# Performance work log

Hardware: AMD Instinct MI355X
Metric: run time of the kernel (lower is better)

## Reference

```python
import jax, jax.numpy as jnp
import numpy as np

C = 128; D_STATE = 16; D_CONV = 4; EXPAND = 2
DI = EXPAND * C          # 256 inner dim
DT_RANK = (C + 15) // 16 # 8
NM, T, V = 32, 64, 22


def _mamba(x, in_w, conv_w, conv_b, xproj_w, dt_w, dt_b, Alog, Dp, out_w):
    """Standard Mamba block. x: (B, L, C) -> (B, L, C)."""
    B_, L, _ = x.shape
    xz = x @ in_w.T                       # (B, L, 2*DI)
    xi, z = jnp.split(xz, 2, axis=-1)     # each (B, L, DI)
    # causal depthwise conv over L, kernel D_CONV
    K = conv_w.shape[-1]
    xp = jnp.pad(xi, ((0, 0), (K - 1, 0), (0, 0)))
    xc = conv_b + sum(xp[:, k:k + L, :] * conv_w[:, k] for k in range(K))
    xc = jax.nn.silu(xc)
    dbl = xc @ xproj_w.T                  # (B, L, DT_RANK + 2*D_STATE)
    dt, Bm, Cm = jnp.split(dbl, [DT_RANK, DT_RANK + D_STATE], axis=-1)
    dt = jax.nn.softplus(dt @ dt_w.T + dt_b)   # (B, L, DI)
    A = -jnp.exp(Alog)                    # (DI, D_STATE), strictly negative

    def step(h, inp):
        dt_l, B_l, C_l, u_l = inp         # (B,DI) (B,DS) (B,DS) (B,DI)
        dA = jnp.exp(dt_l[:, :, None] * A)             # (B, DI, DS)
        h = dA * h + (dt_l * u_l)[:, :, None] * B_l[:, None, :]
        y = jnp.einsum('bds,bs->bd', h, C_l)
        return h, y

    h0 = jnp.zeros((B_, DI, D_STATE), x.dtype)
    xs = (jnp.moveaxis(dt, 1, 0), jnp.moveaxis(Bm, 1, 0),
          jnp.moveaxis(Cm, 1, 0), jnp.moveaxis(xc, 1, 0))
    _, ys = jax.lax.scan(step, h0, xs)    # ys: (L, B, DI)
    y = jnp.moveaxis(ys, 0, 1) + xc * Dp  # skip connection
    y = y * jax.nn.silu(z)
    return y @ out_w.T                    # (B, L, C)


def setup_inputs() -> dict:
    key = jax.random.key(0)
    ks = jax.random.split(key, 40)
    i = [0]
    def nrm(shape, s=0.05):
        i[0] += 1
        return jax.random.normal(ks[i[0]], shape, jnp.float32) * s
    inp = {"x": jax.random.normal(ks[0], (NM, C, T, V), jnp.float32)}
    for p in ("f", "b"):
        inp[p + "_in_w"] = nrm((2 * DI, C))
        inp[p + "_conv_w"] = nrm((DI, D_CONV), 0.2)
        inp[p + "_conv_b"] = nrm((DI,))
        inp[p + "_xproj_w"] = nrm((DT_RANK + 2 * D_STATE, DI))
        inp[p + "_dt_w"] = nrm((DI, DT_RANK), 0.1)
        inp[p + "_dt_b"] = nrm((DI,), 0.1)
        i[0] += 1
        inp[p + "_Alog"] = jax.random.uniform(ks[i[0]], (DI, D_STATE), jnp.float32)
        inp[p + "_D"] = nrm((DI,), 1.0)
        inp[p + "_out_w"] = nrm((C, DI))
    inp["fuse_w"] = nrm((C, 2 * C))
    inp["ln_w"] = jnp.ones((C,), jnp.float32)
    inp["ln_b"] = jnp.zeros((C,), jnp.float32)
    return inp


def reference(x, f_in_w, f_conv_w, f_conv_b, f_xproj_w, f_dt_w, f_dt_b, f_Alog, f_D, f_out_w,
              b_in_w, b_conv_w, b_conv_b, b_xproj_w, b_dt_w, b_dt_b, b_Alog, b_D, b_out_w,
              fuse_w, ln_w, ln_b):
    nm, c, t, v = x.shape
    xs = jnp.transpose(x, (0, 2, 3, 1)).reshape(nm * t, v, c)   # (B, V, C)
    fwd = _mamba(xs, f_in_w, f_conv_w, f_conv_b, f_xproj_w, f_dt_w, f_dt_b, f_Alog, f_D, f_out_w)
    bwd = _mamba(xs[:, ::-1, :], b_in_w, b_conv_w, b_conv_b, b_xproj_w, b_dt_w, b_dt_b, b_Alog, b_D, b_out_w)[:, ::-1, :]
    y = jnp.concatenate([fwd, bwd], axis=-1) @ fuse_w.T         # (B, V, C)
    mu = y.mean(-1, keepdims=True)
    var = y.var(-1, keepdims=True)
    y = (y - mu) / jnp.sqrt(var + 1e-5) * ln_w + ln_b
    return jnp.transpose(y.reshape(nm, t, v, c), (0, 3, 1, 2))  # (NM, C, T, V)
```

## Files before the change

### kernel.cpp

```cpp
#include <hip/hip_runtime.h>
#include <hip/hip_bf16.h>
#include <math.h>

namespace {

typedef unsigned short u16;
typedef unsigned int u32;

constexpr int LSEQ = 22, CD = 128, DI = 256, TDIM = 64;

constexpr int XS_LD = 136;
constexpr int XI_LD = 264;
constexpr int Z_LD  = 264;
constexpr int Y2_LD = 132;

constexpr int O_DT0 = 0;
constexpr int O_DT1 = 352;
constexpr int O_BC0 = 704;
constexpr int O_BC1 = 2112;
constexpr int O_XS  = 0;
constexpr int O_XI0 = 3520;
constexpr int O_XI1 = 9328;
constexpr int O_Z0  = 15136;
constexpr int O_Z1  = 20944;
constexpr int POOLN = 26752;

constexpr int WS_F_IN_HI = 0;
constexpr int WS_F_IN_LO = 65536;
constexpr int WS_B_IN_HI = 131072;
constexpr int WS_B_IN_LO = 196608;
constexpr int WS_F_OUT   = 262144;
constexpr int WS_B_OUT   = 294912;
constexpr int WS_FUSE    = 327680;
constexpr int WS_F_XP_HI = 360448;
constexpr int WS_F_XP_LO = 372736;
constexpr int WS_B_XP_HI = 385024;
constexpr int WS_B_XP_LO = 397312;
constexpr int WS_TOTAL   = 409600;

typedef __attribute__((ext_vector_type(8))) short bf16x8;
typedef __attribute__((ext_vector_type(4))) float f32x4;

__device__ __forceinline__ u16 f2bf(float f) {
  __bf16 b = (__bf16)f;
  return *reinterpret_cast<u16*>(&b);
}
__device__ __forceinline__ float bf2f(u16 h) {
  return __uint_as_float(((u32)h) << 16);
}
__device__ __forceinline__ float sigm(float x) { return 1.0f / (1.0f + __expf(-x)); }

__global__ void prep_weights(const float* __restrict__ f_in, const float* __restrict__ b_in,
                             const float* __restrict__ f_xp, const float* __restrict__ b_xp,
                             u16* __restrict__ ws) {
  int i = blockIdx.x * 256 + threadIdx.x;
  if (i >= WS_TOTAL) return;
  u16 r = 0;
  if (i < WS_F_IN_LO) {
    r = f2bf(f_in[i]);
  } else if (i < WS_B_IN_HI) {
    float v = f_in[i - WS_F_IN_LO];
    r = f2bf(v - bf2f(f2bf(v)));
  } else if (i < WS_B_IN_LO) {
    r = f2bf(b_in[i - WS_B_IN_HI]);
  } else if (i < WS_F_OUT) {
    float v = b_in[i - WS_B_IN_LO];
    r = f2bf(v - bf2f(f2bf(v)));
  } else if (i < WS_F_XP_HI) {
    r = 0;
  } else if (i < WS_F_XP_LO) {
    int j = i - WS_F_XP_HI, n = j >> 8, k = j & 255;
    r = (n < 40) ? f2bf(f_xp[n * 256 + k]) : (u16)0;
  } else if (i < WS_B_XP_HI) {
    int j = i - WS_F_XP_LO, n = j >> 8, k = j & 255;
    if (n < 40) { float v = f_xp[n * 256 + k]; r = f2bf(v - bf2f(f2bf(v))); } else r = 0;
  } else if (i < WS_B_XP_LO) {
    int j = i - WS_B_XP_HI, n = j >> 8, k = j & 255;
    r = (n < 40) ? f2bf(b_xp[n * 256 + k]) : (u16)0;
  } else {
    int j = i - WS_B_XP_LO, n = j >> 8, k = j & 255;
    if (n < 40) { float v = b_xp[n * 256 + k]; r = f2bf(v - bf2f(f2bf(v))); } else r = 0;
  }
  ws[i] = r;
}

__global__ void prep_fold(const float* __restrict__ f_out, const float* __restrict__ b_out,
                          const float* __restrict__ fuse, u16* __restrict__ ws) {
  int i = blockIdx.x * 256 + threadIdx.x;
  int half = i >> 15;
  int j = i & 32767;
  int c = j >> 8, d = j & 255;
  const float* ow = half ? b_out : f_out;
  const float* fw = fuse + c * 256 + half * 128;
  float acc = 0.f;
#pragma unroll 4
  for (int k = 0; k < 128; ++k) acc = fmaf(fw[k], ow[k * 256 + d], acc);
  ws[(half ? WS_B_OUT : WS_F_OUT) + c * 256 + d] = f2bf(acc);
}

__global__ __launch_bounds__(512, 4) void spatial_mamba_kernel(
    const float* __restrict__ x,
    const float* __restrict__ f_conv_w, const float* __restrict__ f_conv_b,
    const float* __restrict__ f_dt_w, const float* __restrict__ f_dt_b,
    const float* __restrict__ f_Alog, const float* __restrict__ f_D,
    const float* __restrict__ b_conv_w, const float* __restrict__ b_conv_b,
    const float* __restrict__ b_dt_w, const float* __restrict__ b_dt_b,
    const float* __restrict__ b_Alog, const float* __restrict__ b_D,
    const float* __restrict__ ln_w, const float* __restrict__ ln_b,
    const u16* __restrict__ ws,
    float* __restrict__ out)
{
  __shared__ __align__(16) u16 pool[POOLN];

  u16* xs = pool + O_XS;
  float* y2 = (float*)(pool + O_Z0);
  float* mu_s = (float*)pool;
  float* rs_s = mu_s + LSEQ;

  const int tid = threadIdx.x;
  const int wv = tid >> 6, ln = tid & 63, lr = ln & 15, lg = ln >> 4;
  const int blk = blockIdx.x;
  const int nm = blk / TDIM, t = blk - nm * TDIM;
  const size_t base = (size_t)nm * CD * (TDIM * LSEQ) + (size_t)t * LSEQ;

  const int ra0 = (lr < LSEQ) ? lr : (LSEQ - 1);
  const int ra1 = (16 + lr < LSEQ) ? (16 + lr) : (LSEQ - 1);
  const int rb0 = (LSEQ - 1) - lr;
  const int rb1 = (lr < 6) ? (5 - lr) : 0;

  for (int idx = tid; idx < LSEQ * CD; idx += 512) {
    int c = idx / LSEQ, v = idx - c * LSEQ;
    xs[v * XS_LD + c] = f2bf(x[base + (size_t)c * (TDIM * LSEQ) + v]);
  }
  __syncthreads();

  {
    bf16x8 afr[2][4];
#pragma unroll
    for (int kt = 0; kt < 4; ++kt) {
      afr[0][kt] = *(const bf16x8*)&xs[ra0 * XS_LD + kt * 32 + lg * 8];
      afr[1][kt] = *(const bf16x8*)&xs[ra1 * XS_LD + kt * 32 + lg * 8];
    }
#pragma unroll
    for (int dir = 0; dir < 2; ++dir) {
      const u16* ih = ws + (dir ? WS_B_IN_HI : WS_F_IN_HI);
      const u16* il = ws + (dir ? WS_B_IN_LO : WS_F_IN_LO);
      f32x4 acc[2][4];
#pragma unroll
      for (int m = 0; m < 2; ++m)
#pragma unroll
        for (int n = 0; n < 4; ++n) acc[m][n] = f32x4{0.f, 0.f, 0.f, 0.f};
#pragma unroll
      for (int kt = 0; kt < 4; ++kt) {
#pragma unroll
        for (int n = 0; n < 4; ++n) {
          const int off = (wv * 64 + n * 16 + lr) * 128 + kt * 32 + lg * 8;
          bf16x8 bh = *(const bf16x8*)(ih + off);
          bf16x8 bl = *(const bf16x8*)(il + off);
          acc[0][n] = __builtin_amdgcn_mfma_f32_16x16x32_bf16(afr[0][kt], bh, acc[0][n], 0, 0, 0);
          acc[0][n] = __builtin_amdgcn_mfma_f32_16x16x32_bf16(afr[0][kt], bl, acc[0][n], 0, 0, 0);
          acc[1][n] = __builtin_amdgcn_mfma_f32_16x16x32_bf16(afr[1][kt], bh, acc[1][n], 0, 0, 0);
          acc[1][n] = __builtin_amdgcn_mfma_f32_16x16x32_bf16(afr[1][kt], bl, acc[1][n], 0, 0, 0);
        }
      }
      u16* dst = pool + ((wv < 4) ? (dir ? O_XI1 : O_XI0) : (dir ? O_Z1 : O_Z0));
      const int cb = (wv & 3) * 64;
#pragma unroll
      for (int m = 0; m < 2; ++m)
#pragma unroll
        for (int n = 0; n < 4; ++n)
#pragma unroll
          for (int j = 0; j < 4; ++j) {
            int row = 16 * m + lg * 4 + j;
            if (row < LSEQ) {
              int rr = dir ? (LSEQ - 1 - row) : row;
              dst[rr * XI_LD + cb + n * 16 + lr] = f2bf(acc[m][n][j]);
            }
          }
    }
  }
  __syncthreads();

  {
    const int dir = tid >> 8, d = tid & 255;
    const float* cw = dir ? b_conv_w : f_conv_w;
    const float* cbp = dir ? b_conv_b : f_conv_b;
    u16* xiD = pool + (dir ? O_XI1 : O_XI0);
    float4 w4 = *(const float4*)(cw + d * 4);
    float bb = cbp[d];
    float w0 = 0.f, w1 = 0.f, w2 = 0.f;
#pragma unroll
    for (int l = 0; l < LSEQ; ++l) {
      float w3 = bf2f(xiD[l * XI_LD + d]);
      float a = fmaf(w0, w4.x, bb);
      a = fmaf(w1, w4.y, a);
      a = fmaf(w2, w4.z, a);
      a = fmaf(w3, w4.w, a);
      float s = a * sigm(a);
      xiD[l * XI_LD + d] = f2bf(s);
      w0 = w1; w1 = w2; w2 = w3;
    }
  }
  __syncthreads();

  for (int tt = wv; tt < 12; tt += 8) {
    const int dir = tt / 6, r = tt - dir * 6, mt = r / 3, nt = r - mt * 3;
    const u16* xph = ws + (dir ? WS_B_XP_HI : WS_F_XP_HI);
    const u16* xpl = ws + (dir ? WS_B_XP_LO : WS_F_XP_LO);
    const u16* xcD = pool + (dir ? O_XI1 : O_XI0);
    const int ra = (mt * 16 + lr < LSEQ) ? (mt * 16 + lr) : (LSEQ - 1);
    f32x4 acc = f32x4{0.f, 0.f, 0.f, 0.f};
    const u16* bh_p = xph + (nt * 16 + lr) * 256 + lg * 8;
    const u16* bl_p = xpl + (nt * 16 + lr) * 256 + lg * 8;
#pragma unroll
    for (int kt = 0; kt < 8; ++kt) {
      bf16x8 a  = *(const bf16x8*)&xcD[ra * XI_LD + kt * 32 + lg * 8];
      bf16x8 bh = *(const bf16x8*)(bh_p + kt * 32);
      bf16x8 bl = *(const bf16x8*)(bl_p + kt * 32);
      acc = __builtin_amdgcn_mfma_f32_16x16x32_bf16(a, bh, acc, 0, 0, 0);
      acc = __builtin_amdgcn_mfma_f32_16x16x32_bf16(a, bl, acc, 0, 0, 0);
    }
    const int col = nt * 16 + lr;
    float* dtD = ((float*)pool) + (dir ? (O_DT1 / 2) : 0);
    float* bcD = ((float*)pool) + (dir ? (O_BC1 / 2) : (O_BC0 / 2));
#pragma unroll
    for (int j = 0; j < 4; ++j) {
      int row = mt * 16 + lg * 4 + j;
      if (row < LSEQ) {
        if (col < 8) dtD[row * 8 + col] = acc[j];
        else if (col < 40) bcD[row * 32 + (col - 8)] = acc[j];
      }
    }
  }
  __syncthreads();

  {
    const int dir = tid >> 8, d = tid & 255;
    const float* dtw  = dir ? b_dt_w : f_dt_w;
    const float* dtb  = dir ? b_dt_b : f_dt_b;
    const float* Alog = dir ? b_Alog : f_Alog;
    const float* Dp   = dir ? b_D : f_D;
    const float* dtD  = ((const float*)pool) + (dir ? (O_DT1 / 2) : 0);
    const float* bcD  = ((const float*)pool) + (dir ? (O_BC1 / 2) : (O_BC0 / 2));
    const u16* zD  = pool + (dir ? O_Z1 : O_Z0);
    u16* yD = pool + (dir ? O_XI1 : O_XI0);

    float4 dw0 = *(const float4*)(dtw + d * 8);
    float4 dw1 = *(const float4*)(dtw + d * 8 + 4);
    const float dtbv = dtb[d];
    float Av[16];
#pragma unroll
    for (int s4 = 0; s4 < 4; ++s4) {
      float4 a = *(const float4*)(Alog + d * 16 + s4 * 4);
      Av[s4 * 4 + 0] = -__expf(a.x);
      Av[s4 * 4 + 1] = -__expf(a.y);
      Av[s4 * 4 + 2] = -__expf(a.z);
      Av[s4 * 4 + 3] = -__expf(a.w);
    }
    const float Dd = Dp[d];
    float h[16];
#pragma unroll
    for (int s = 0; s < 16; ++s) h[s] = 0.f;
    for (int l = 0; l < LSEQ; ++l) {
      float4 q0 = *(const float4*)(dtD + l * 8);
      float4 q1 = *(const float4*)(dtD + l * 8 + 4);
      float sdt = dtbv;
      sdt = fmaf(q0.x, dw0.x, sdt); sdt = fmaf(q0.y, dw0.y, sdt);
      sdt = fmaf(q0.z, dw0.z, sdt); sdt = fmaf(q0.w, dw0.w, sdt);
      sdt = fmaf(q1.x, dw1.x, sdt); sdt = fmaf(q1.y, dw1.y, sdt);
      sdt = fmaf(q1.z, dw1.z, sdt); sdt = fmaf(q1.w, dw1.w, sdt);
      float dtv = (sdt > 20.f) ? sdt : __logf(1.f + __expf(sdt));
      float u = bf2f(yD[l * XI_LD + d]);
      float du = dtv * u;
      float4 b0 = *(const float4*)(bcD + l * 32);
      float4 b1 = *(const float4*)(bcD + l * 32 + 4);
      float4 b2 = *(const float4*)(bcD + l * 32 + 8);
      float4 b3 = *(const float4*)(bcD + l * 32 + 12);
      float4 c0 = *(const float4*)(bcD + l * 32 + 16);
      float4 c1 = *(const float4*)(bcD + l * 32 + 20);
      float4 c2 = *(const float4*)(bcD + l * 32 + 24);
      float4 c3 = *(const float4*)(bcD + l * 32 + 28);
      float acc = 0.f;
#define SC(s, bv, cv) { float dA = __expf(dtv * Av[s]); \
      h[s] = fmaf(dA, h[s], du * (bv)); \
      acc = fmaf(h[s], (cv), acc); }
      SC(0, b0.x, c0.x) SC(1, b0.y, c0.y) SC(2, b0.z, c0.z) SC(3, b0.w, c0.w)
      SC(4, b1.x, c1.x) SC(5, b1.y, c1.y) SC(6, b1.z, c1.z) SC(7, b1.w, c1.w)
      SC(8, b2.x, c2.x) SC(9, b2.y, c2.y) SC(10, b2.z, c2.z) SC(11, b2.w, c2.w)
      SC(12, b3.x, c3.x) SC(13, b3.y, c3.y) SC(14, b3.z, c3.z) SC(15, b3.w, c3.w)
#undef SC
      float zv = bf2f(zD[l * Z_LD + d]);
      float yo = fmaf(u, Dd, acc) * zv * sigm(zv);
      yD[l * XI_LD + d] = f2bf(yo);
    }
  }
  __syncthreads();

  {
    f32x4 acc[2] = {f32x4{0.f, 0.f, 0.f, 0.f}, f32x4{0.f, 0.f, 0.f, 0.f}};
    {
      const u16* wp = ws + WS_F_OUT;
      const u16* yD = pool + O_XI0;
#pragma unroll
      for (int kt = 0; kt < 8; ++kt) {
        bf16x8 b  = *(const bf16x8*)(wp + (wv * 16 + lr) * 256 + kt * 32 + lg * 8);
        bf16x8 a0 = *(const bf16x8*)&yD[ra0 * XI_LD + kt * 32 + lg * 8];
        bf16x8 a1 = *(const bf16x8*)&yD[ra1 * XI_LD + kt * 32 + lg * 8];
        acc[0] = __builtin_amdgcn_mfma_f32_16x16x32_bf16(a0, b, acc[0], 0, 0, 0);
        acc[1] = __builtin_amdgcn_mfma_f32_16x16x32_bf16(a1, b, acc[1], 0, 0, 0);
      }
    }
    {
      const u16* wp = ws + WS_B_OUT;
      const u16* yD = pool + O_XI1;
#pragma unroll
      for (int kt = 0; kt < 8; ++kt) {
        bf16x8 b  = *(const bf16x8*)(wp + (wv * 16 + lr) * 256 + kt * 32 + lg * 8);
        bf16x8 a0 = *(const bf16x8*)&yD[rb0 * XI_LD + kt * 32 + lg * 8];
        bf16x8 a1 = *(const bf16x8*)&yD[rb1 * XI_LD + kt * 32 + lg * 8];
        acc[0] = __builtin_amdgcn_mfma_f32_16x16x32_bf16(a0, b, acc[0], 0, 0, 0);
        acc[1] = __builtin_amdgcn_mfma_f32_16x16x32_bf16(a1, b, acc[1], 0, 0, 0);
      }
    }
#pragma unroll
    for (int m = 0; m < 2; ++m)
#pragma unroll
      for (int j = 0; j < 4; ++j) {
        int row = 16 * m + lg * 4 + j;
        if (row < LSEQ) y2[row * Y2_LD + wv * 16 + lr] = acc[m][j];
      }
  }
  __syncthreads();

  {
    for (int l = wv; l < LSEQ; l += 8) {
      float v1 = y2[l * Y2_LD + ln];
      float v2 = y2[l * Y2_LD + 64 + ln];
      float s = v1 + v2;
      float sq = v1 * v1 + v2 * v2;
#pragma unroll
      for (int m = 1; m < 64; m <<= 1) {
        s  += __shfl_xor(s, m, 64);
        sq += __shfl_xor(sq, m, 64);
      }
      if (ln == 0) {
        float mu = s * (1.0f / 128.0f);
        float var = sq * (1.0f / 128.0f) - mu * mu;
        mu_s[l] = mu;
        rs_s[l] = rsqrtf(var + 1e-5f);
      }
    }
  }
  __syncthreads();

  for (int idx = tid; idx < LSEQ * CD; idx += 512) {
    int c = idx / LSEQ, v = idx - c * LSEQ;
    float yv = y2[v * Y2_LD + c];
    float o = (yv - mu_s[v]) * rs_s[v] * ln_w[c] + ln_b[c];
    out[base + (size_t)c * (TDIM * LSEQ) + v] = o;
  }
}

}

extern "C" void kernel_launch(void* const* d_in, const int* in_sizes, int n_in,
                              void* d_out, int out_size, void* d_ws, size_t ws_size,
                              hipStream_t stream) {
  (void)in_sizes; (void)n_in; (void)ws_size; (void)out_size;
  const float* p[22];
  for (int i = 0; i < 22; ++i) p[i] = (const float*)d_in[i];
  u16* ws = (u16*)d_ws;
  prep_weights<<<dim3((WS_TOTAL + 255) / 256), dim3(256), 0, stream>>>(
      p[1], p[10], p[4], p[13], ws);
  prep_fold<<<dim3(256), dim3(256), 0, stream>>>(p[9], p[18], p[19], ws);
  spatial_mamba_kernel<<<dim3(32 * 64), dim3(512), 0, stream>>>(
      p[0],
      p[2], p[3], p[5], p[6], p[7], p[8],
      p[11], p[12], p[14], p[15], p[16], p[17],
      p[20], p[21], ws, (float*)d_out);
}
```

Measured before the change: 280.9 us.

## Split fused kernel into per-direction scan blocks and a separate fold+layernorm kernel

The single 512-thread kernel, which handled both scan directions per sequence, becomes two kernels. The first runs 256-thread blocks, one per (sequence, direction), doing in-projection, conv, x-projection and the selective scan, and writes y as bf16 to the workspace. The second kernel reads both directions back, applies the folded out/fuse projection and the layernorm. The split aims for smaller blocks with less shared memory and higher occupancy. It also software-pipelines the conv load and the softplus of dt. The cost is an extra global round trip of the y tensor, a duplicated x load per direction, and an extra launch.

```diff
diff --git a/kernel.cpp b/kernel.cpp
--- a/kernel.cpp
+++ b/kernel.cpp
@@ -11,19 +11,14 @@
 
 constexpr int XS_LD = 136;
 constexpr int XI_LD = 264;
-constexpr int Z_LD  = 264;
 constexpr int Y2_LD = 132;
 
-constexpr int O_DT0 = 0;
-constexpr int O_DT1 = 352;
-constexpr int O_BC0 = 704;
-constexpr int O_BC1 = 2112;
-constexpr int O_XS  = 0;
-constexpr int O_XI0 = 3520;
-constexpr int O_XI1 = 9328;
-constexpr int O_Z0  = 15136;
-constexpr int O_Z1  = 20944;
-constexpr int POOLN = 26752;
+constexpr int K1_XS = 0;
+constexpr int K1_XI = 2992;
+constexpr int K1_Z  = 8800;
+constexpr int K1_N  = 14608;
+
+constexpr int K2_N  = 11616;
 
 constexpr int WS_F_IN_HI = 0;
 constexpr int WS_F_IN_LO = 65536;
@@ -37,6 +32,7 @@
 constexpr int WS_B_XP_HI = 385024;
 constexpr int WS_B_XP_LO = 397312;
 constexpr int WS_TOTAL   = 409600;
+constexpr int WS_Y       = 409600;
 
 typedef __attribute__((ext_vector_type(8))) short bf16x8;
 typedef __attribute__((ext_vector_type(4))) float f32x4;
@@ -98,7 +94,7 @@
   ws[(half ? WS_B_OUT : WS_F_OUT) + c * 256 + d] = f2bf(acc);
 }
 
-__global__ __launch_bounds__(512, 4) void spatial_mamba_kernel(
+__global__ __launch_bounds__(256, 5) void mamba_scan_kernel(
     const float* __restrict__ x,
     const float* __restrict__ f_conv_w, const float* __restrict__ f_conv_b,
     const float* __restrict__ f_dt_w, const float* __restrict__ f_dt_b,
@@ -106,29 +102,25 @@
     const float* __restrict__ b_conv_w, const float* __restrict__ b_conv_b,
     const float* __restrict__ b_dt_w, const float* __restrict__ b_dt_b,
     const float* __restrict__ b_Alog, const float* __restrict__ b_D,
-    const float* __restrict__ ln_w, const float* __restrict__ ln_b,
-    const u16* __restrict__ ws,
-    float* __restrict__ out)
+    u16* __restrict__ ws)
 {
-  __shared__ __align__(16) u16 pool[POOLN];
-
-  u16* xs = pool + O_XS;
-  float* y2 = (float*)(pool + O_Z0);
-  float* mu_s = (float*)pool;
-  float* rs_s = mu_s + LSEQ;
+  __shared__ __align__(16) u16 pool[K1_N];
+
+  u16* xs  = pool + K1_XS;
+  u16* xiD = pool + K1_XI;
+  u16* zD  = pool + K1_Z;
 
   const int tid = threadIdx.x;
   const int wv = tid >> 6, ln = tid & 63, lr = ln & 15, lg = ln >> 4;
-  const int blk = blockIdx.x;
-  const int nm = blk / TDIM, t = blk - nm * TDIM;
+  const int bid = blockIdx.x;
+  const int b = bid >> 1, dir = bid & 1;
+  const int nm = b / TDIM, t = b - nm * TDIM;
   const size_t base = (size_t)nm * CD * (TDIM * LSEQ) + (size_t)t * LSEQ;
 
   const int ra0 = (lr < LSEQ) ? lr : (LSEQ - 1);
   const int ra1 = (16 + lr < LSEQ) ? (16 + lr) : (LSEQ - 1);
-  const int rb0 = (LSEQ - 1) - lr;
-  const int rb1 = (lr < 6) ? (5 - lr) : 0;
-
-  for (int idx = tid; idx < LSEQ * CD; idx += 512) {
+
+  for (int idx = tid; idx < LSEQ * CD; idx += 256) {
     int c = idx / LSEQ, v = idx - c * LSEQ;
     xs[v * XS_LD + c] = f2bf(x[base + (size_t)c * (TDIM * LSEQ) + v]);
   }
@@ -141,10 +133,12 @@
       afr[0][kt] = *(const bf16x8*)&xs[ra0 * XS_LD + kt * 32 + lg * 8];
       afr[1][kt] = *(const bf16x8*)&xs[ra1 * XS_LD + kt * 32 + lg * 8];
     }
-#pragma unroll
-    for (int dir = 0; dir < 2; ++dir) {
-      const u16* ih = ws + (dir ? WS_B_IN_HI : WS_F_IN_HI);
-      const u16* il = ws + (dir ? WS_B_IN_LO : WS_F_IN_LO);
+    const u16* ih = ws + (dir ? WS_B_IN_HI : WS_F_IN_HI);
+    const u16* il = ws + (dir ? WS_B_IN_LO : WS_F_IN_LO);
+    u16* dst = (wv < 2) ? xiD : zD;
+    const int cb0 = (wv & 1) * 128;
+#pragma unroll
+    for (int half = 0; half < 2; ++half) {
       f32x4 acc[2][4];
 #pragma unroll
       for (int m = 0; m < 2; ++m)
@@ -154,7 +148,7 @@
       for (int kt = 0; kt < 4; ++kt) {
 #pragma unroll
         for (int n = 0; n < 4; ++n) {
-          const int off = (wv * 64 + n * 16 + lr) * 128 + kt * 32 + lg * 8;
+          const int off = (wv * 128 + (half * 4 + n) * 16 + lr) * 128 + kt * 32 + lg * 8;
           bf16x8 bh = *(const bf16x8*)(ih + off);
           bf16x8 bl = *(const bf16x8*)(il + off);
           acc[0][n] = __builtin_amdgcn_mfma_f32_16x16x32_bf16(afr[0][kt], bh, acc[0][n], 0, 0, 0);
@@ -163,8 +157,6 @@
           acc[1][n] = __builtin_amdgcn_mfma_f32_16x16x32_bf16(afr[1][kt], bl, acc[1][n], 0, 0, 0);
         }
       }
-      u16* dst = pool + ((wv < 4) ? (dir ? O_XI1 : O_XI0) : (dir ? O_Z1 : O_Z0));
-      const int cb = (wv & 3) * 64;
 #pragma unroll
       for (int m = 0; m < 2; ++m)
 #pragma unroll
@@ -174,7 +166,7 @@
             int row = 16 * m + lg * 4 + j;
             if (row < LSEQ) {
               int rr = dir ? (LSEQ - 1 - row) : row;
-              dst[rr * XI_LD + cb + n * 16 + lr] = f2bf(acc[m][n][j]);
+              dst[rr * XI_LD + cb0 + half * 64 + n * 16 + lr] = f2bf(acc[m][n][j]);
             }
           }
     }
@@ -182,16 +174,17 @@
   __syncthreads();
 
   {
-    const int dir = tid >> 8, d = tid & 255;
-    const float* cw = dir ? b_conv_w : f_conv_w;
+    const int d = tid;
+    const float* cw  = dir ? b_conv_w : f_conv_w;
     const float* cbp = dir ? b_conv_b : f_conv_b;
-    u16* xiD = pool + (dir ? O_XI1 : O_XI0);
     float4 w4 = *(const float4*)(cw + d * 4);
     float bb = cbp[d];
     float w0 = 0.f, w1 = 0.f, w2 = 0.f;
+    float nxt = bf2f(xiD[d]);
 #pragma unroll
     for (int l = 0; l < LSEQ; ++l) {
-      float w3 = bf2f(xiD[l * XI_LD + d]);
+      float w3 = nxt;
+      if (l + 1 < LSEQ) nxt = bf2f(xiD[(l + 1) * XI_LD + d]);
       float a = fmaf(w0, w4.x, bb);
       a = fmaf(w1, w4.y, a);
       a = fmaf(w2, w4.z, a);
@@ -203,26 +196,25 @@
   }
   __syncthreads();
 
-  for (int tt = wv; tt < 12; tt += 8) {
-    const int dir = tt / 6, r = tt - dir * 6, mt = r / 3, nt = r - mt * 3;
+  for (int tt = wv; tt < 6; tt += 4) {
+    const int mt = tt / 3, nt = tt - mt * 3;
     const u16* xph = ws + (dir ? WS_B_XP_HI : WS_F_XP_HI);
     const u16* xpl = ws + (dir ? WS_B_XP_LO : WS_F_XP_LO);
-    const u16* xcD = pool + (dir ? O_XI1 : O_XI0);
-    const int ra = (mt * 16 + lr < LSEQ) ? (mt * 16 + lr) : (LSEQ - 1);
+    const int raa = (mt * 16 + lr < LSEQ) ? (mt * 16 + lr) : (LSEQ - 1);
     f32x4 acc = f32x4{0.f, 0.f, 0.f, 0.f};
     const u16* bh_p = xph + (nt * 16 + lr) * 256 + lg * 8;
     const u16* bl_p = xpl + (nt * 16 + lr) * 256 + lg * 8;
 #pragma unroll
     for (int kt = 0; kt < 8; ++kt) {
-      bf16x8 a  = *(const bf16x8*)&xcD[ra * XI_LD + kt * 32 + lg * 8];
+      bf16x8 a  = *(const bf16x8*)&xiD[raa * XI_LD + kt * 32 + lg * 8];
       bf16x8 bh = *(const bf16x8*)(bh_p + kt * 32);
       bf16x8 bl = *(const bf16x8*)(bl_p + kt * 32);
       acc = __builtin_amdgcn_mfma_f32_16x16x32_bf16(a, bh, acc, 0, 0, 0);
       acc = __builtin_amdgcn_mfma_f32_16x16x32_bf16(a, bl, acc, 0, 0, 0);
     }
     const int col = nt * 16 + lr;
-    float* dtD = ((float*)pool) + (dir ? (O_DT1 / 2) : 0);
-    float* bcD = ((float*)pool) + (dir ? (O_BC1 / 2) : (O_BC0 / 2));
+    float* dtD = (float*)pool;
+    float* bcD = ((float*)pool) + 176;
 #pragma unroll
     for (int j = 0; j < 4; ++j) {
       int row = mt * 16 + lg * 4 + j;
@@ -235,15 +227,13 @@
   __syncthreads();
 
   {
-    const int dir = tid >> 8, d = tid & 255;
+    const int d = tid;
     const float* dtw  = dir ? b_dt_w : f_dt_w;
     const float* dtb  = dir ? b_dt_b : f_dt_b;
     const float* Alog = dir ? b_Alog : f_Alog;
     const float* Dp   = dir ? b_D : f_D;
-    const float* dtD  = ((const float*)pool) + (dir ? (O_DT1 / 2) : 0);
-    const float* bcD  = ((const float*)pool) + (dir ? (O_BC1 / 2) : (O_BC0 / 2));
-    const u16* zD  = pool + (dir ? O_Z1 : O_Z0);
-    u16* yD = pool + (dir ? O_XI1 : O_XI0);
+    const float* dtD  = (const float*)pool;
+    const float* bcD  = ((const float*)pool) + 176;
 
     float4 dw0 = *(const float4*)(dtw + d * 8);
     float4 dw1 = *(const float4*)(dtw + d * 8 + 4);
@@ -258,10 +248,9 @@
       Av[s4 * 4 + 3] = -__expf(a.w);
     }
     const float Dd = Dp[d];
-    float h[16];
-#pragma unroll
-    for (int s = 0; s < 16; ++s) h[s] = 0.f;
-    for (int l = 0; l < LSEQ; ++l) {
+    u16* wsY = ws + WS_Y + (size_t)b * 11264 + dir * 5632;
+
+    auto softp = [&](int l) -> float {
       float4 q0 = *(const float4*)(dtD + l * 8);
       float4 q1 = *(const float4*)(dtD + l * 8 + 4);
       float sdt = dtbv;
@@ -269,8 +258,16 @@
       sdt = fmaf(q0.z, dw0.z, sdt); sdt = fmaf(q0.w, dw0.w, sdt);
       sdt = fmaf(q1.x, dw1.x, sdt); sdt = fmaf(q1.y, dw1.y, sdt);
       sdt = fmaf(q1.z, dw1.z, sdt); sdt = fmaf(q1.w, dw1.w, sdt);
-      float dtv = (sdt > 20.f) ? sdt : __logf(1.f + __expf(sdt));
-      float u = bf2f(yD[l * XI_LD + d]);
+      return (sdt > 20.f) ? sdt : __logf(1.f + __expf(sdt));
+    };
+
+    float h[16];
+#pragma unroll
+    for (int s = 0; s < 16; ++s) h[s] = 0.f;
+    float dtv = softp(0);
+    for (int l = 0; l < LSEQ; ++l) {
+      float dtv_n = (l + 1 < LSEQ) ? softp(l + 1) : 0.f;
+      float u = bf2f(xiD[l * XI_LD + d]);
       float du = dtv * u;
       float4 b0 = *(const float4*)(bcD + l * 32);
       float4 b1 = *(const float4*)(bcD + l * 32 + 4);
@@ -289,71 +286,95 @@
       SC(8, b2.x, c2.x) SC(9, b2.y, c2.y) SC(10, b2.z, c2.z) SC(11, b2.w, c2.w)
       SC(12, b3.x, c3.x) SC(13, b3.y, c3.y) SC(14, b3.z, c3.z) SC(15, b3.w, c3.w)
 #undef SC
-      float zv = bf2f(zD[l * Z_LD + d]);
+      float zv = bf2f(zD[l * XI_LD + d]);
       float yo = fmaf(u, Dd, acc) * zv * sigm(zv);
-      yD[l * XI_LD + d] = f2bf(yo);
-    }
-  }
-  __syncthreads();
-
-  {
-    f32x4 acc[2] = {f32x4{0.f, 0.f, 0.f, 0.f}, f32x4{0.f, 0.f, 0.f, 0.f}};
-    {
-      const u16* wp = ws + WS_F_OUT;
-      const u16* yD = pool + O_XI0;
-#pragma unroll
-      for (int kt = 0; kt < 8; ++kt) {
-        bf16x8 b  = *(const bf16x8*)(wp + (wv * 16 + lr) * 256 + kt * 32 + lg * 8);
-        bf16x8 a0 = *(const bf16x8*)&yD[ra0 * XI_LD + kt * 32 + lg * 8];
-        bf16x8 a1 = *(const bf16x8*)&yD[ra1 * XI_LD + kt * 32 + lg * 8];
-        acc[0] = __builtin_amdgcn_mfma_f32_16x16x32_bf16(a0, b, acc[0], 0, 0, 0);
-        acc[1] = __builtin_amdgcn_mfma_f32_16x16x32_bf16(a1, b, acc[1], 0, 0, 0);
+      wsY[(dir ? (LSEQ - 1 - l) : l) * DI + d] = f2bf(yo);
+      dtv = dtv_n;
+    }
+  }
+}
+
+__global__ __launch_bounds__(256, 6) void fold_ln_kernel(
+    const float* __restrict__ ln_w, const float* __restrict__ ln_b,
+    const u16* __restrict__ ws, float* __restrict__ out)
+{
+  __shared__ __align__(16) u16 pool[K2_N];
+
+  const int tid = threadIdx.x;
+  const int wv = tid >> 6, ln = tid & 63, lr = ln & 15, lg = ln >> 4;
+  const int b = blockIdx.x;
+  const int nm = b / TDIM, t = b - nm * TDIM;
+  const size_t base = (size_t)nm * CD * (TDIM * LSEQ) + (size_t)t * LSEQ;
+  const u16* wsY = ws + WS_Y + (size_t)b * 11264;
+
+  for (int idx = tid; idx < 2 * LSEQ * 32; idx += 256) {
+    int dirc = idx / 704, r = idx - dirc * 704;
+    int l = r >> 5, ch = (r & 31) * 8;
+    *(bf16x8*)&pool[dirc * 5808 + l * XI_LD + ch] =
+        *(const bf16x8*)(wsY + dirc * 5632 + l * 256 + ch);
+  }
+  __syncthreads();
+
+  const int ra0 = (lr < LSEQ) ? lr : (LSEQ - 1);
+  const int ra1 = (16 + lr < LSEQ) ? (16 + lr) : (LSEQ - 1);
+
+  f32x4 acc[2][2];
+#pragma unroll
+  for (int m = 0; m < 2; ++m)
+#pragma unroll
+    for (int n = 0; n < 2; ++n) acc[m][n] = f32x4{0.f, 0.f, 0.f, 0.f};
+#pragma unroll
+  for (int dirc = 0; dirc < 2; ++dirc) {
+    const u16* wp = ws + (dirc ? WS_B_OUT : WS_F_OUT);
+    const u16* yD = pool + dirc * 5808;
+#pragma unroll
+    for (int kt = 0; kt < 8; ++kt) {
+      bf16x8 a0 = *(const bf16x8*)&yD[ra0 * XI_LD + kt * 32 + lg * 8];
+      bf16x8 a1 = *(const bf16x8*)&yD[ra1 * XI_LD + kt * 32 + lg * 8];
+#pragma unroll
+      for (int n = 0; n < 2; ++n) {
+        bf16x8 bw = *(const bf16x8*)(wp + (wv * 32 + n * 16 + lr) * 256 + kt * 32 + lg * 8);
+        acc[0][n] = __builtin_amdgcn_mfma_f32_16x16x32_bf16(a0, bw, acc[0][n], 0, 0, 0);
+        acc[1][n] = __builtin_amdgcn_mfma_f32_16x16x32_bf16(a1, bw, acc[1][n], 0, 0, 0);
       }
     }
-    {
-      const u16* wp = ws + WS_B_OUT;
-      const u16* yD = pool + O_XI1;
-#pragma unroll
-      for (int kt = 0; kt < 8; ++kt) {
-        bf16x8 b  = *(const bf16x8*)(wp + (wv * 16 + lr) * 256 + kt * 32 + lg * 8);
-        bf16x8 a0 = *(const bf16x8*)&yD[rb0 * XI_LD + kt * 32 + lg * 8];
-        bf16x8 a1 = *(const bf16x8*)&yD[rb1 * XI_LD + kt * 32 + lg * 8];
-        acc[0] = __builtin_amdgcn_mfma_f32_16x16x32_bf16(a0, b, acc[0], 0, 0, 0);
-        acc[1] = __builtin_amdgcn_mfma_f32_16x16x32_bf16(a1, b, acc[1], 0, 0, 0);
-      }
-    }
-#pragma unroll
-    for (int m = 0; m < 2; ++m)
+  }
+  __syncthreads();
+
+  float* y2 = (float*)pool;
+#pragma unroll
+  for (int m = 0; m < 2; ++m)
+#pragma unroll
+    for (int n = 0; n < 2; ++n)
 #pragma unroll
       for (int j = 0; j < 4; ++j) {
         int row = 16 * m + lg * 4 + j;
-        if (row < LSEQ) y2[row * Y2_LD + wv * 16 + lr] = acc[m][j];
+        if (row < LSEQ) y2[row * Y2_LD + wv * 32 + n * 16 + lr] = acc[m][n][j];
       }
-  }
-  __syncthreads();
-
-  {
-    for (int l = wv; l < LSEQ; l += 8) {
-      float v1 = y2[l * Y2_LD + ln];
-      float v2 = y2[l * Y2_LD + 64 + ln];
-      float s = v1 + v2;
-      float sq = v1 * v1 + v2 * v2;
-#pragma unroll
-      for (int m = 1; m < 64; m <<= 1) {
-        s  += __shfl_xor(s, m, 64);
-        sq += __shfl_xor(sq, m, 64);
-      }
-      if (ln == 0) {
-        float mu = s * (1.0f / 128.0f);
-        float var = sq * (1.0f / 128.0f) - mu * mu;
-        mu_s[l] = mu;
-        rs_s[l] = rsqrtf(var + 1e-5f);
-      }
-    }
-  }
-  __syncthreads();
-
-  for (int idx = tid; idx < LSEQ * CD; idx += 512) {
+  __syncthreads();
+
+  float* mu_s = (float*)(pool + 5808);
+  float* rs_s = mu_s + LSEQ;
+  for (int l = wv; l < LSEQ; l += 4) {
+    float v1 = y2[l * Y2_LD + ln];
+    float v2 = y2[l * Y2_LD + 64 + ln];
+    float s = v1 + v2;
+    float sq = v1 * v1 + v2 * v2;
+#pragma unroll
+    for (int m = 1; m < 64; m <<= 1) {
+      s  += __shfl_xor(s, m, 64);
+      sq += __shfl_xor(sq, m, 64);
+    }
+    if (ln == 0) {
+      float mu = s * (1.0f / 128.0f);
+      float var = sq * (1.0f / 128.0f) - mu * mu;
+      mu_s[l] = mu;
+      rs_s[l] = rsqrtf(var + 1e-5f);
+    }
+  }
+  __syncthreads();
+
+  for (int idx = tid; idx < LSEQ * CD; idx += 256) {
     int c = idx / LSEQ, v = idx - c * LSEQ;
     float yv = y2[v * Y2_LD + c];
     float o = (yv - mu_s[v]) * rs_s[v] * ln_w[c] + ln_b[c];
@@ -373,9 +394,11 @@
   prep_weights<<<dim3((WS_TOTAL + 255) / 256), dim3(256), 0, stream>>>(
       p[1], p[10], p[4], p[13], ws);
   prep_fold<<<dim3(256), dim3(256), 0, stream>>>(p[9], p[18], p[19], ws);
-  spatial_mamba_kernel<<<dim3(32 * 64), dim3(512), 0, stream>>>(
+  mamba_scan_kernel<<<dim3(32 * 64 * 2), dim3(256), 0, stream>>>(
       p[0],
       p[2], p[3], p[5], p[6], p[7], p[8],
       p[11], p[12], p[14], p[15], p[16], p[17],
+      ws);
+  fold_ln_kernel<<<dim3(32 * 64), dim3(256), 0, stream>>>(
       p[20], p[21], ws, (float*)d_out);
 }
```

New measurement: 299.0 us. 6.4% more time.
